# Optimization experiments

Measured on AMD Instinct MI355X. Metric: run time of the kernel, lower is better.

Reference implementation:

```python
import jax, jax.numpy as jnp
import numpy as np

B, N, E = 128, 16384, 1048576
H, C = 512, 10


def setup_inputs() -> dict:
    key = jax.random.key(0)
    ks = jax.random.split(key, 10)
    x = jax.random.normal(ks[0], (B, N), dtype=jnp.float32)
    edge_index = jax.random.randint(ks[1], (2, E), 0, N, dtype=jnp.int64)
    edge_weight = jax.random.uniform(ks[2], (E,), dtype=jnp.float32)
    W1 = jax.random.normal(ks[3], (H, N), dtype=jnp.float32) * (1.0 / np.sqrt(N))
    b1 = jax.random.normal(ks[4], (H,), dtype=jnp.float32) * 0.01
    W2 = jax.random.normal(ks[5], (H, H), dtype=jnp.float32) * (1.0 / np.sqrt(H))
    b2 = jax.random.normal(ks[6], (H,), dtype=jnp.float32) * 0.01
    Wfc = jax.random.normal(ks[7], (C, H), dtype=jnp.float32) * (1.0 / np.sqrt(H))
    bfc = jax.random.normal(ks[8], (C,), dtype=jnp.float32) * 0.01
    return {"x": x, "edge_index": edge_index, "edge_weight": edge_weight,
            "W1": W1, "b1": b1, "W2": W2, "b2": b2, "Wfc": Wfc, "bfc": bfc}


def _sgconv_propagate(x, edge_index, edge_weight):
    """One GCN-normalized propagation (SGConv K=1, lin.weight==1, no bias).
    Batched edge offsets in the original == same operator applied per row.
    x: (B, N); edge_index: (2, E); edge_weight: (E,). Returns (B, N).
    """
    n = x.shape[1]
    src, dst = edge_index[0], edge_index[1]
    loop = jnp.arange(n, dtype=src.dtype)
    src_f = jnp.concatenate([src, loop])
    dst_f = jnp.concatenate([dst, loop])
    w_f = jnp.concatenate([edge_weight, jnp.ones((n,), x.dtype)])  # self-loop weight 1
    deg = jax.ops.segment_sum(w_f, dst_f, num_segments=n)  # in-degree (col)
    dinv = jnp.where(deg > 0, jax.lax.rsqrt(jnp.maximum(deg, 1e-12)), 0.0)
    norm = dinv[src_f] * w_f * dinv[dst_f]  # (E+N,)
    msgs = x[:, src_f] * norm  # (B, E+N) gather + scale
    return jax.ops.segment_sum(msgs.T, dst_f, num_segments=n).T  # scatter-add -> (B, N)


def reference(x, edge_index, edge_weight, W1, b1, W2, b2, Wfc, bfc):
    h = _sgconv_propagate(x, edge_index, edge_weight)  # diffusion (B, N)
    h = jax.nn.relu(h @ W1.T + b1)  # Linear(N->H) + ReLU
    h = jax.nn.relu(h @ W2.T + b2)  # Linear(H->H) + ReLU
    return h @ Wfc.T + bfc  # fc (H->C), softmax=False, dropout=0 (eval)
```

## Files before the change

### kernel.cpp

```cpp
#include <hip/hip_runtime.h>
#include <hip/hip_bf16.h>
#include <stdint.h>

#define B_DIM 128
#define N_DIM 16384
#define E_DIM 1048576
#define H_DIM 512
#define C_DIM 10
#define NWG 256
#define CHUNK (E_DIM / NWG)
#define NWORD8 (N_DIM / 4)
#define NGRP 8
#define WPG (NWG / NGRP)
#define SPLITK 64
#define KC (N_DIM / SPLITK)

typedef __attribute__((ext_vector_type(8))) short short8;
typedef __attribute__((ext_vector_type(4))) float f32x4;

__device__ __forceinline__ uint32_t f2bf(float f) {
    uint32_t u = __float_as_uint(f);
    return (u + 0x7fffu + ((u >> 16) & 1u)) >> 16;
}

__global__ void __launch_bounds__(256) k_thist(const float* __restrict__ x,
                                               float* __restrict__ xT,
                                               const int* __restrict__ dst,
                                               uint32_t* __restrict__ slab) {
    __shared__ uint32_t ls[NWORD8];
    int bid = blockIdx.x, t = threadIdx.x;
    {
        float* ftile = (float*)ls;
        int tx = t & 31, tyb = t >> 5;
        for (int tile = bid * 8; tile < bid * 8 + 8; tile++) {
            int bx = tile >> 2, by = tile & 3;
#pragma unroll
            for (int r = 0; r < 4; r++) {
                int ty = r * 8 + tyb;
                ftile[ty * 33 + tx] = x[(size_t)(by * 32 + ty) * N_DIM + bx * 32 + tx];
            }
            __syncthreads();
#pragma unroll
            for (int r = 0; r < 4; r++) {
                int ty = r * 8 + tyb;
                xT[(size_t)(bx * 32 + ty) * B_DIM + by * 32 + tx] = ftile[tx * 33 + ty];
            }
            __syncthreads();
        }
    }
#pragma unroll
    for (int i = 0; i < NWORD8 / 256; i++) ls[i * 256 + t] = 0;
    __syncthreads();
#pragma unroll
    for (int i = 0; i < CHUNK / 256; i++) {
        int d = dst[bid * CHUNK + i * 256 + t];
        atomicAdd(&ls[d >> 2], 1u << ((d & 3) << 3));
    }
    __syncthreads();
#pragma unroll
    for (int i = 0; i < NWORD8 / 256; i++)
        slab[(size_t)bid * NWORD8 + i * 256 + t] = ls[i * 256 + t];
}

__global__ void __launch_bounds__(128) k_scanA8(uint32_t* __restrict__ slab,
                                                uint32_t* __restrict__ grp) {
    int b = blockIdx.x;
    int g = b >> 5;
    int j = (b & 31) * 128 + threadIdx.x;
    uint32_t run = 0;
    for (int w = g * WPG; w < (g + 1) * WPG; w++) {
        uint32_t c = slab[(size_t)w * NWORD8 + j];
        slab[(size_t)w * NWORD8 + j] = run;
        run += c;
    }
    grp[(size_t)g * NWORD8 + j] = run;
}

__global__ void __launch_bounds__(1024) k_scanBC8(uint32_t* __restrict__ grp,
                                                  int* __restrict__ offs) {
    __shared__ uint32_t part[1024];
    int t = threadIdx.x;
    uint32_t tw[4];
    int loc[16];
    uint32_t s = 0;
    int k = 0;
#pragma unroll
    for (int i = 0; i < 4; i++) {
        int j = t * 4 + i;
        uint32_t run = 0;
#pragma unroll
        for (int g = 0; g < NGRP; g++) {
            uint32_t c = grp[(size_t)g * NWORD8 + j];
            grp[(size_t)g * NWORD8 + j] = run;
            run += c;
        }
        tw[i] = run;
#pragma unroll
        for (int b4 = 0; b4 < 4; b4++) {
            loc[k] = (int)s;
            s += (tw[i] >> (b4 * 8)) & 0xffu;
            k++;
        }
    }
    part[t] = s;
    __syncthreads();
    for (int off = 1; off < 1024; off <<= 1) {
        uint32_t v = (t >= off) ? part[t - off] : 0;
        __syncthreads();
        part[t] += v;
        __syncthreads();
    }
    uint32_t ex = (t == 0) ? 0 : part[t - 1];
#pragma unroll
    for (int i = 0; i < 16; i++) offs[t * 16 + i] = (int)(ex + loc[i]);
    if (t == 1023) offs[N_DIM] = (int)part[1023];
}

__global__ void __launch_bounds__(256) k_place2(const int* __restrict__ src,
                                                const int* __restrict__ dst,
                                                const float* __restrict__ ew,
                                                const uint32_t* __restrict__ slab,
                                                const uint32_t* __restrict__ grp,
                                                const int* __restrict__ offs,
                                                int2* __restrict__ packed) {
    __shared__ uint32_t cur[N_DIM];
    int w = blockIdx.x, t = threadIdx.x;
    int g = w >> 5;
#pragma unroll
    for (int i = 0; i < NWORD8 / 256; i++) {
        int j = i * 256 + t;
        uint32_t pv = slab[(size_t)w * NWORD8 + j];
        uint32_t gv = grp[(size_t)g * NWORD8 + j];
        int4 o = *(const int4*)&offs[4 * j];
        cur[4 * j + 0] = (uint32_t)o.x + (gv & 0xffu) + (pv & 0xffu);
        cur[4 * j + 1] = (uint32_t)o.y + ((gv >> 8) & 0xffu) + ((pv >> 8) & 0xffu);
        cur[4 * j + 2] = (uint32_t)o.z + ((gv >> 16) & 0xffu) + ((pv >> 16) & 0xffu);
        cur[4 * j + 3] = (uint32_t)o.w + (gv >> 24) + (pv >> 24);
    }
    __syncthreads();
    int e = w * CHUNK + t;
    int s = src[e], d = dst[e];
    float wv = ew[e];
#pragma unroll
    for (int i = 0; i < CHUNK / 256; i++) {
        int sn = 0, dn = 0;
        float wn = 0.f;
        if (i + 1 < CHUNK / 256) {
            int en = e + 256;
            sn = src[en]; dn = dst[en]; wn = ew[en];
        }
        uint32_t pos = atomicAdd(&cur[d], 1u);
        packed[pos] = make_int2(s, __float_as_int(wv));
        s = sn; d = dn; wv = wn; e += 256;
    }
}

__global__ void __launch_bounds__(256) k_degscale(const int* __restrict__ offs,
                                                  const int2* __restrict__ packed,
                                                  float* __restrict__ dinv,
                                                  const float* __restrict__ xT,
                                                  uint16_t* __restrict__ xTh) {
    int d = blockIdx.x * 4 + (threadIdx.x >> 6);
    int lane = threadIdx.x & 63;
    int e0 = offs[d], e1 = offs[d + 1];
    float s = 0.f;
    for (int e = e0 + lane; e < e1; e += 64)
        s += __int_as_float(packed[e].y);
#pragma unroll
    for (int o = 32; o > 0; o >>= 1) s += __shfl_down(s, o);
    float dv = __shfl(rsqrtf(s + 1.0f), 0);
    if (lane == 0) dinv[d] = dv;
    float2 v = ((const float2*)&xT[(size_t)d * B_DIM])[lane];
    uint32_t b = f2bf(v.x * dv) | (f2bf(v.y * dv) << 16);
    ((uint32_t*)(xTh + (size_t)d * B_DIM))[lane] = b;
}

__global__ void __launch_bounds__(256) k_diffuse(const uint16_t* __restrict__ xTh,
                                                 const int* __restrict__ offs,
                                                 const int2* __restrict__ packed,
                                                 const float* __restrict__ dinv,
                                                 uint16_t* __restrict__ hB) {
    __shared__ uint4 ls[128];
    int wave = threadIdx.x >> 6;
    int d0 = blockIdx.x * 8 + wave * 2;
    int lane = threadIdx.x & 63;
    int g = lane >> 4;
    int colh = lane & 15;
    const uint4* x4 = (const uint4*)xTh;
    int oA = offs[d0], oM = offs[d0 + 1], oB = offs[d0 + 2];
    int eA = oA + lane;
    int2 pA = (eA < oM) ? packed[eA] : make_int2(0, 0);
    int eB = oM + lane;
    int2 pB = (eB < oB) ? packed[eB] : make_int2(0, 0);
    float accA[8], accB[8];
#pragma unroll
    for (int k = 0; k < 8; k++) { accA[k] = 0.f; accB[k] = 0.f; }
    for (int base = oA; base < oM; base += 64) {
        int2 pc = pA;
        int en = base + 64 + lane;
        pA = (en < oM) ? packed[en] : make_int2(0, 0);
#pragma unroll
        for (int i = 0; i < 64; i += 4) {
            int idx = i + g;
            int sx = __shfl(pc.x, idx);
            float nm = __shfl(__int_as_float(pc.y), idx);
            uint4 xs = x4[(size_t)sx * 16 + colh];
            accA[0] = fmaf(nm, __uint_as_float(xs.x << 16), accA[0]);
            accA[1] = fmaf(nm, __uint_as_float(xs.x & 0xffff0000u), accA[1]);
            accA[2] = fmaf(nm, __uint_as_float(xs.y << 16), accA[2]);
            accA[3] = fmaf(nm, __uint_as_float(xs.y & 0xffff0000u), accA[3]);
            accA[4] = fmaf(nm, __uint_as_float(xs.z << 16), accA[4]);
            accA[5] = fmaf(nm, __uint_as_float(xs.z & 0xffff0000u), accA[5]);
            accA[6] = fmaf(nm, __uint_as_float(xs.w << 16), accA[6]);
            accA[7] = fmaf(nm, __uint_as_float(xs.w & 0xffff0000u), accA[7]);
        }
    }
    for (int base = oM; base < oB; base += 64) {
        int2 pc = pB;
        int en = base + 64 + lane;
        pB = (en < oB) ? packed[en] : make_int2(0, 0);
#pragma unroll
        for (int i = 0; i < 64; i += 4) {
            int idx = i + g;
            int sx = __shfl(pc.x, idx);
            float nm = __shfl(__int_as_float(pc.y), idx);
            uint4 xs = x4[(size_t)sx * 16 + colh];
            accB[0] = fmaf(nm, __uint_as_float(xs.x << 16), accB[0]);
            accB[1] = fmaf(nm, __uint_as_float(xs.x & 0xffff0000u), accB[1]);
            accB[2] = fmaf(nm, __uint_as_float(xs.y << 16), accB[2]);
            accB[3] = fmaf(nm, __uint_as_float(xs.y & 0xffff0000u), accB[3]);
            accB[4] = fmaf(nm, __uint_as_float(xs.z << 16), accB[4]);
            accB[5] = fmaf(nm, __uint_as_float(xs.z & 0xffff0000u), accB[5]);
            accB[6] = fmaf(nm, __uint_as_float(xs.w << 16), accB[6]);
            accB[7] = fmaf(nm, __uint_as_float(xs.w & 0xffff0000u), accB[7]);
        }
    }
#pragma unroll
    for (int off = 16; off <= 32; off <<= 1)
#pragma unroll
        for (int k = 0; k < 8; k++) {
            accA[k] += __shfl_xor(accA[k], off);
            accB[k] += __shfl_xor(accB[k], off);
        }
    int who = lane >> 4;
    if (who < 2) {
        int dd = d0 + who;
        float dv = dinv[dd];
        uint4 sv = x4[(size_t)dd * 16 + colh];
        float o[8];
#pragma unroll
        for (int k = 0; k < 8; k++) o[k] = (who == 0) ? accA[k] : accB[k];
        o[0] = (o[0] + __uint_as_float(sv.x << 16)) * dv;
        o[1] = (o[1] + __uint_as_float(sv.x & 0xffff0000u)) * dv;
        o[2] = (o[2] + __uint_as_float(sv.y << 16)) * dv;
        o[3] = (o[3] + __uint_as_float(sv.y & 0xffff0000u)) * dv;
        o[4] = (o[4] + __uint_as_float(sv.z << 16)) * dv;
        o[5] = (o[5] + __uint_as_float(sv.z & 0xffff0000u)) * dv;
        o[6] = (o[6] + __uint_as_float(sv.w << 16)) * dv;
        o[7] = (o[7] + __uint_as_float(sv.w & 0xffff0000u)) * dv;
        uint4 r;
        r.x = f2bf(o[0]) | (f2bf(o[1]) << 16);
        r.y = f2bf(o[2]) | (f2bf(o[3]) << 16);
        r.z = f2bf(o[4]) | (f2bf(o[5]) << 16);
        r.w = f2bf(o[6]) | (f2bf(o[7]) << 16);
        ls[(wave * 2 + who) * 16 + colh] = r;
    }
    __syncthreads();
    int t = threadIdx.x;
    if (t < 128) {
        const uint16_t* l16 = (const uint16_t*)ls;
        uint16_t v0 = l16[0 * 128 + t], v1 = l16[1 * 128 + t];
        uint16_t v2 = l16[2 * 128 + t], v3 = l16[3 * 128 + t];
        uint16_t v4 = l16[4 * 128 + t], v5 = l16[5 * 128 + t];
        uint16_t v6 = l16[6 * 128 + t], v7 = l16[7 * 128 + t];
        uint4 r;
        r.x = (uint32_t)v0 | ((uint32_t)v1 << 16);
        r.y = (uint32_t)v2 | ((uint32_t)v3 << 16);
        r.z = (uint32_t)v4 | ((uint32_t)v5 << 16);
        r.w = (uint32_t)v6 | ((uint32_t)v7 << 16);
        *(uint4*)&hB[(size_t)t * N_DIM + blockIdx.x * 8] = r;
    }
}

__global__ void __launch_bounds__(256) k_gemm1(const float* __restrict__ W1,
                                               const uint16_t* __restrict__ hB,
                                               float* __restrict__ part) {
    int kc = blockIdx.x;
    int mt = blockIdx.y;
    int t = threadIdx.x, w = t >> 6, l = t & 63;
    int lr = l & 15;
    int lk = (l >> 4) * 8;
    int row = mt * 64 + w * 16 + lr;
    int k0 = kc * KC;
    f32x4 acc[8] = {};
    const float* wbase = W1 + (size_t)row * N_DIM + k0 + lk;
    const uint16_t* hbase = hB + k0 + lk;
#pragma unroll 2
    for (int ks = 0; ks < KC; ks += 32) {
        float4 wa = *(const float4*)(wbase + ks);
        float4 wb = *(const float4*)(wbase + ks + 4);
        short8 bf[8];
#pragma unroll
        for (int c = 0; c < 8; c++)
            bf[c] = *(const short8*)(hbase + (size_t)(c * 16 + lr) * N_DIM + ks);
        float wv0 = wa.x, wv1 = wa.y, wv2 = wa.z, wv3 = wa.w;
        float wv4 = wb.x, wv5 = wb.y, wv6 = wb.z, wv7 = wb.w;
        short8 ahi, alo;
        uint32_t h0;
        h0 = f2bf(wv0); ahi[0] = (short)h0; alo[0] = (short)f2bf(wv0 - __uint_as_float(h0 << 16));
        h0 = f2bf(wv1); ahi[1] = (short)h0; alo[1] = (short)f2bf(wv1 - __uint_as_float(h0 << 16));
        h0 = f2bf(wv2); ahi[2] = (short)h0; alo[2] = (short)f2bf(wv2 - __uint_as_float(h0 << 16));
        h0 = f2bf(wv3); ahi[3] = (short)h0; alo[3] = (short)f2bf(wv3 - __uint_as_float(h0 << 16));
        h0 = f2bf(wv4); ahi[4] = (short)h0; alo[4] = (short)f2bf(wv4 - __uint_as_float(h0 << 16));
        h0 = f2bf(wv5); ahi[5] = (short)h0; alo[5] = (short)f2bf(wv5 - __uint_as_float(h0 << 16));
        h0 = f2bf(wv6); ahi[6] = (short)h0; alo[6] = (short)f2bf(wv6 - __uint_as_float(h0 << 16));
        h0 = f2bf(wv7); ahi[7] = (short)h0; alo[7] = (short)f2bf(wv7 - __uint_as_float(h0 << 16));
#pragma unroll
        for (int c = 0; c < 8; c++) {
            acc[c] = __builtin_amdgcn_mfma_f32_16x16x32_bf16(ahi, bf[c], acc[c], 0, 0, 0);
            acc[c] = __builtin_amdgcn_mfma_f32_16x16x32_bf16(alo, bf[c], acc[c], 0, 0, 0);
        }
    }
    float* pbase = part + (size_t)kc * (H_DIM * B_DIM)
                 + (size_t)(mt * 64 + w * 16 + (l >> 4) * 4) * B_DIM + lr;
#pragma unroll
    for (int c = 0; c < 8; c++)
#pragma unroll
        for (int r = 0; r < 4; r++)
            pbase[(size_t)r * B_DIM + c * 16] = acc[c][r];
}

__global__ void __launch_bounds__(256) k_reduce1(const float* __restrict__ part,
                                                 const float* __restrict__ b1,
                                                 float* __restrict__ h1) {
    __shared__ float ls[128][9];
    int bid = blockIdx.x;
    int t = threadIdx.x;
    int j0 = bid * 8;
    int jl = t >> 5;
    int b0 = (t & 31) * 4;
    float bias = b1[j0 + jl];
    float4 s = make_float4(bias, bias, bias, bias);
    const float* pb = part + (size_t)j0 * B_DIM + t * 4;
#pragma unroll
    for (int c = 0; c < SPLITK; c++) {
        float4 v = *(const float4*)(pb + (size_t)c * (H_DIM * B_DIM));
        s.x += v.x; s.y += v.y; s.z += v.z; s.w += v.w;
    }
    ls[b0 + 0][jl] = fmaxf(s.x, 0.f);
    ls[b0 + 1][jl] = fmaxf(s.y, 0.f);
    ls[b0 + 2][jl] = fmaxf(s.z, 0.f);
    ls[b0 + 3][jl] = fmaxf(s.w, 0.f);
    __syncthreads();
    int b = t >> 1;
    int off = (t & 1) * 4;
    float4 w = make_float4(ls[b][off], ls[b][off + 1], ls[b][off + 2], ls[b][off + 3]);
    *(float4*)&h1[(size_t)b * H_DIM + j0 + off] = w;
}

__global__ void __launch_bounds__(1024) k_tail23(const float* __restrict__ W2,
                                                 const float* __restrict__ b2,
                                                 const float* __restrict__ Wfc,
                                                 const float* __restrict__ bfc,
                                                 const float* __restrict__ h1,
                                                 float* __restrict__ out) {
    __shared__ float h2s[H_DIM];
    int b = blockIdx.x;
    int t = threadIdx.x;
    int w = t >> 6;
    int l = t & 63;
    const float* hb = h1 + (size_t)b * H_DIM;
    float hv[8];
#pragma unroll
    for (int k = 0; k < 8; k++) hv[k] = hb[k * 64 + l];
#pragma unroll
    for (int it = 0; it < 4; it++) {
        int j0 = w * 32 + it * 8;
        float outv = 0.f;
#pragma unroll
        for (int jj = 0; jj < 8; jj++) {
            const float* wrow = W2 + (size_t)(j0 + jj) * H_DIM;
            float a = 0.f;
#pragma unroll
            for (int k = 0; k < 8; k++) a = fmaf(wrow[k * 64 + l], hv[k], a);
#pragma unroll
            for (int o = 1; o < 64; o <<= 1) a += __shfl_xor(a, o);
            if (l == jj) outv = a;
        }
        if (l < 8) h2s[j0 + l] = fmaxf(outv + b2[j0 + l], 0.f);
    }
    __syncthreads();
    if (w == 0) {
        float hv2[8];
#pragma unroll
        for (int k = 0; k < 8; k++) hv2[k] = h2s[k * 64 + l];
        float outv = 0.f;
#pragma unroll
        for (int c = 0; c < C_DIM; c++) {
            const float* wrow = Wfc + (size_t)c * H_DIM;
            float a = 0.f;
#pragma unroll
            for (int k = 0; k < 8; k++) a = fmaf(wrow[k * 64 + l], hv2[k], a);
#pragma unroll
            for (int o = 1; o < 64; o <<= 1) a += __shfl_xor(a, o);
            if (l == c) outv = a;
        }
        if (l < C_DIM) out[b * C_DIM + l] = outv + bfc[l];
    }
}

extern "C" void kernel_launch(void* const* d_in, const int* in_sizes, int n_in,
                              void* d_out, int out_size, void* d_ws, size_t ws_size,
                              hipStream_t stream) {
    const float* x   = (const float*)d_in[0];
    const int*   ei  = (const int*)d_in[1];
    const float* ew  = (const float*)d_in[2];
    const float* W1  = (const float*)d_in[3];
    const float* b1  = (const float*)d_in[4];
    const float* W2  = (const float*)d_in[5];
    const float* b2  = (const float*)d_in[6];
    const float* Wfc = (const float*)d_in[7];
    const float* bfc = (const float*)d_in[8];
    float* out = (float*)d_out;

    const int* src = ei;
    const int* dst = ei + E_DIM;

    char* ws = (char*)d_ws;
    size_t off = 0;
    auto alloc = [&](size_t bytes) -> void* {
        void* p = ws + off;
        off = (off + bytes + 255) & ~(size_t)255;
        return p;
    };
    float* xT     = (float*)alloc((size_t)N_DIM * B_DIM * 4);
    uint16_t* xTh = (uint16_t*)alloc((size_t)N_DIM * B_DIM * 2);
    int2*  packed = (int2*) alloc((size_t)E_DIM * 8);
    size_t sort_bytes = (size_t)NWG * NWORD8 * 4 + (size_t)NGRP * NWORD8 * 4;
    size_t part_bytes = (size_t)SPLITK * H_DIM * B_DIM * 4;
    char* scratch = (char*)alloc(sort_bytes > part_bytes ? sort_bytes : part_bytes);
    float* h1     = (float*)alloc((size_t)H_DIM * B_DIM * 4);
    int*   offs   = (int*)  alloc((size_t)(N_DIM + 1) * 4);
    float* dinv   = (float*)alloc((size_t)N_DIM * 4);
    uint16_t* hB  = (uint16_t*)alloc((size_t)B_DIM * N_DIM * 2);
    uint32_t* slab = (uint32_t*)scratch;
    uint32_t* grp  = (uint32_t*)(scratch + (size_t)NWG * NWORD8 * 4);
    float* part    = (float*)scratch;
    if (off > ws_size) return;

    k_thist<<<NWG, 256, 0, stream>>>(x, xT, dst, slab);
    k_scanA8<<<NWG, 128, 0, stream>>>(slab, grp);
    k_scanBC8<<<1, 1024, 0, stream>>>(grp, offs);
    k_place2<<<NWG, 256, 0, stream>>>(src, dst, ew, slab, grp, offs, packed);
    k_degscale<<<N_DIM / 4, 256, 0, stream>>>(offs, packed, dinv, xT, xTh);
    k_diffuse<<<N_DIM / 8, 256, 0, stream>>>(xTh, offs, packed, dinv, hB);
    k_gemm1<<<dim3(SPLITK, H_DIM / 64), 256, 0, stream>>>(W1, hB, part);
    k_reduce1<<<64, 256, 0, stream>>>(part, b1, h1);
    k_tail23<<<B_DIM, 1024, 0, stream>>>(W2, b2, Wfc, bfc, h1, out);
}
```

Baseline: 122.6 us.

## Fuse x transpose into degree-scale kernel, drop fp32 transposed intermediate

The fp32 transpose of x moves out of the histogram kernel and into the degree/scale kernel. That kernel now loads a 16-node by 128-batch tile of x directly through shared memory, scales it by dinv and writes bf16. This removes the 8 MB fp32 xT write and its later re-read, and shrinks the histogram kernel. The tradeoff is that the x reads in degscale are strided: each thread group reads 16 contiguous floats per batch row, which gives short 64-byte segments.

```diff
diff --git a/kernel.cpp b/kernel.cpp
--- a/kernel.cpp
+++ b/kernel.cpp
@@ -23,31 +23,10 @@
     return (u + 0x7fffu + ((u >> 16) & 1u)) >> 16;
 }
 
-__global__ void __launch_bounds__(256) k_thist(const float* __restrict__ x,
-                                               float* __restrict__ xT,
-                                               const int* __restrict__ dst,
+__global__ void __launch_bounds__(256) k_hist1(const int* __restrict__ dst,
                                                uint32_t* __restrict__ slab) {
     __shared__ uint32_t ls[NWORD8];
     int bid = blockIdx.x, t = threadIdx.x;
-    {
-        float* ftile = (float*)ls;
-        int tx = t & 31, tyb = t >> 5;
-        for (int tile = bid * 8; tile < bid * 8 + 8; tile++) {
-            int bx = tile >> 2, by = tile & 3;
-#pragma unroll
-            for (int r = 0; r < 4; r++) {
-                int ty = r * 8 + tyb;
-                ftile[ty * 33 + tx] = x[(size_t)(by * 32 + ty) * N_DIM + bx * 32 + tx];
-            }
-            __syncthreads();
-#pragma unroll
-            for (int r = 0; r < 4; r++) {
-                int ty = r * 8 + tyb;
-                xT[(size_t)(bx * 32 + ty) * B_DIM + by * 32 + tx] = ftile[tx * 33 + ty];
-            }
-            __syncthreads();
-        }
-    }
 #pragma unroll
     for (int i = 0; i < NWORD8 / 256; i++) ls[i * 256 + t] = 0;
     __syncthreads();
@@ -157,22 +136,49 @@
 
 __global__ void __launch_bounds__(256) k_degscale(const int* __restrict__ offs,
                                                   const int2* __restrict__ packed,
+                                                  const float* __restrict__ x,
                                                   float* __restrict__ dinv,
-                                                  const float* __restrict__ xT,
                                                   uint16_t* __restrict__ xTh) {
-    int d = blockIdx.x * 4 + (threadIdx.x >> 6);
-    int lane = threadIdx.x & 63;
-    int e0 = offs[d], e1 = offs[d + 1];
-    float s = 0.f;
-    for (int e = e0 + lane; e < e1; e += 64)
-        s += __int_as_float(packed[e].y);
-#pragma unroll
-    for (int o = 32; o > 0; o >>= 1) s += __shfl_down(s, o);
-    float dv = __shfl(rsqrtf(s + 1.0f), 0);
-    if (lane == 0) dinv[d] = dv;
-    float2 v = ((const float2*)&xT[(size_t)d * B_DIM])[lane];
-    uint32_t b = f2bf(v.x * dv) | (f2bf(v.y * dv) << 16);
-    ((uint32_t*)(xTh + (size_t)d * B_DIM))[lane] = b;
+    __shared__ float tile[16][132];
+    __shared__ float dvs[16];
+    int bid = blockIdx.x;
+    int d0 = bid * 16;
+    int t = threadIdx.x;
+    int wave = t >> 6, lane = t & 63;
+#pragma unroll
+    for (int i = 0; i < 4; i++) {
+        int dl = wave * 4 + i;
+        int d = d0 + dl;
+        int e0 = offs[d], e1 = offs[d + 1];
+        float s = 0.f;
+        for (int e = e0 + lane; e < e1; e += 64)
+            s += __int_as_float(packed[e].y);
+#pragma unroll
+        for (int o = 32; o > 0; o >>= 1) s += __shfl_down(s, o);
+        if (lane == 0) {
+            float dv = rsqrtf(s + 1.0f);
+            dvs[dl] = dv;
+            dinv[d] = dv;
+        }
+    }
+    int dl = t & 15, bg = t >> 4;
+#pragma unroll
+    for (int i = 0; i < 8; i++) {
+        int b = bg * 8 + i;
+        tile[dl][b] = x[(size_t)b * N_DIM + d0 + dl];
+    }
+    __syncthreads();
+    int r = t >> 4, cg = t & 15;
+    float dv = dvs[r];
+    uint4 w;
+    uint32_t* wp = (uint32_t*)&w;
+#pragma unroll
+    for (int j = 0; j < 4; j++) {
+        float a = tile[r][cg * 8 + j * 2] * dv;
+        float b = tile[r][cg * 8 + j * 2 + 1] * dv;
+        wp[j] = f2bf(a) | (f2bf(b) << 16);
+    }
+    *(uint4*)&xTh[(size_t)(d0 + r) * B_DIM + cg * 8] = w;
 }
 
 __global__ void __launch_bounds__(256) k_diffuse(const uint16_t* __restrict__ xTh,
@@ -433,7 +439,6 @@
         off = (off + bytes + 255) & ~(size_t)255;
         return p;
     };
-    float* xT     = (float*)alloc((size_t)N_DIM * B_DIM * 4);
     uint16_t* xTh = (uint16_t*)alloc((size_t)N_DIM * B_DIM * 2);
     int2*  packed = (int2*) alloc((size_t)E_DIM * 8);
     size_t sort_bytes = (size_t)NWG * NWORD8 * 4 + (size_t)NGRP * NWORD8 * 4;
@@ -448,11 +453,11 @@
     float* part    = (float*)scratch;
     if (off > ws_size) return;
 
-    k_thist<<<NWG, 256, 0, stream>>>(x, xT, dst, slab);
+    k_hist1<<<NWG, 256, 0, stream>>>(dst, slab);
     k_scanA8<<<NWG, 128, 0, stream>>>(slab, grp);
     k_scanBC8<<<1, 1024, 0, stream>>>(grp, offs);
     k_place2<<<NWG, 256, 0, stream>>>(src, dst, ew, slab, grp, offs, packed);
-    k_degscale<<<N_DIM / 4, 256, 0, stream>>>(offs, packed, dinv, xT, xTh);
+    k_degscale<<<N_DIM / 16, 256, 0, stream>>>(offs, packed, x, dinv, xTh);
     k_diffuse<<<N_DIM / 8, 256, 0, stream>>>(xTh, offs, packed, dinv, hB);
     k_gemm1<<<dim3(SPLITK, H_DIM / 64), 256, 0, stream>>>(W1, hB, part);
     k_reduce1<<<64, 256, 0, stream>>>(part, b1, h1);
```

Measured after the change: 121.0 us. No clear change (-1.3%).
